# Performance work log

Measured on AMD Instinct MI355X. Metric: run time of the kernel, lower is better.

Reference implementation:

```python
import jax, jax.numpy as jnp
import numpy as np

B, T, H, W_SP, C_IN, C_OUT, K = 4, 16, 64, 64, 64, 64, 3
BN_EPS = 1e-3  # keras BatchNormalization default epsilon


def _conv(x, k):
    # x: [N, H, W, Cin], k: [kh, kw, Cin, Cout], 'same' padding, stride 1
    return jax.lax.conv_general_dilated(
        x, k, window_strides=(1, 1), padding='SAME',
        dimension_numbers=('NHWC', 'HWIO', 'NHWC'))


def _hard_sigmoid(x):
    # keras hard_sigmoid: clip(0.2*x + 0.5, 0, 1)
    return jnp.clip(0.2 * x + 0.5, 0.0, 1.0)


def setup_inputs() -> dict:
    key = jax.random.key(0)
    ks = jax.random.split(key, 4)
    x = jax.random.normal(ks[0], (B, T, H, W_SP, C_IN), dtype=jnp.float32)
    # ConvLSTM2D weights: input kernel [kh,kw,Cin,4*Cout], recurrent kernel
    # [kh,kw,Cout,4*Cout], bias [4*Cout]; gate order i, f, c, o (keras).
    W = jax.random.normal(ks[1], (K, K, C_IN, 4 * C_OUT), dtype=jnp.float32) * 0.05
    U = jax.random.normal(ks[2], (K, K, C_OUT, 4 * C_OUT), dtype=jnp.float32) * 0.05
    b = jax.random.normal(ks[3], (4 * C_OUT,), dtype=jnp.float32) * 0.05
    # BatchNormalization (inference mode since training=False)
    gamma = jnp.ones((C_OUT,), jnp.float32)
    beta = jnp.zeros((C_OUT,), jnp.float32)
    moving_mean = jnp.zeros((C_OUT,), jnp.float32)
    moving_var = jnp.ones((C_OUT,), jnp.float32)
    return {'input_tensor': x, 'W': W, 'U': U, 'b': b, 'gamma': gamma,
            'beta': beta, 'moving_mean': moving_mean, 'moving_var': moving_var}


def reference(input_tensor, W, U, b, gamma, beta, moving_mean, moving_var):
    x = input_tensor
    Bn, Tn, Hn, Wn, Cin = x.shape
    C = U.shape[2]
    # Precompute input-to-gate convolutions for all timesteps at once.
    zx = _conv(x.reshape(Bn * Tn, Hn, Wn, Cin), W)
    zx = zx.reshape(Bn, Tn, Hn, Wn, 4 * C) + b
    zx = jnp.moveaxis(zx, 1, 0)  # [T, B, H, W, 4C]

    h0 = jnp.zeros((Bn, Hn, Wn, C), x.dtype)
    c0 = jnp.zeros((Bn, Hn, Wn, C), x.dtype)

    def step(carry, zx_t):
        h, c = carry
        z = zx_t + _conv(h, U)
        zi, zf, zg, zo = jnp.split(z, 4, axis=-1)
        i = _hard_sigmoid(zi)
        f = _hard_sigmoid(zf)
        g = jnp.tanh(zg)           # activation='tanh'
        o = _hard_sigmoid(zo)      # recurrent_activation='hard_sigmoid'
        c_new = f * c + i * g
        h_new = o * jnp.tanh(c_new)
        return (h_new, c_new), h_new

    _, hs = jax.lax.scan(step, (h0, c0), zx)  # hs: [T, B, H, W, C]
    y = jnp.moveaxis(hs, 0, 1)                # [B, T, H, W, C]

    # BatchNorm inference on channel axis
    y = (y - moving_mean) * jax.lax.rsqrt(moving_var + BN_EPS) * gamma + beta

    # MaxPooling3D pool_size=(1,2,2), strides default = pool_size, padding='same'
    y = jax.lax.reduce_window(y, -jnp.inf, jax.lax.max,
                              window_dimensions=(1, 1, 2, 2, 1),
                              window_strides=(1, 1, 2, 2, 1),
                              padding='SAME')
    return y  # [B, T, H/2, W/2, C]
```

## Files before the change

### kernel.cpp

```cpp
#include <hip/hip_runtime.h>
#include <hip/hip_fp16.h>
#include <math.h>

#define BB   4
#define TT   16
#define HH   64
#define WW   64
#define CC   64
#define CO4  256
#define BN_EPS 1e-3f

typedef _Float16 f16;
typedef f16  f16x8 __attribute__((ext_vector_type(8)));
typedef float f32x4 __attribute__((ext_vector_type(4)));

#define INPAD_BYTES (BB * 66 * 66 * 128 * 2)
#define CST_BYTES   (BB * 64 * 64 * 64 * 4)
#define Z_BYTES     (BB * 64 * 64 * 256 * 4)
#define OFF_CST   INPAD_BYTES
#define OFF_Z     (INPAD_BYTES + CST_BYTES)
#define OFF_WT    (OFF_Z + Z_BYTES)

__global__ __launch_bounds__(256) void prep_wt_kernel(
    const float* __restrict__ W, const float* __restrict__ U,
    f16* __restrict__ wt)
{
    int idx = blockIdx.x * 256 + threadIdx.x;
    if (idx >= 256 * 1152) return;
    int n = idx / 1152;
    int k = idx - n * 1152;
    int tap = k >> 7;
    int ci  = k & 127;
    float v = (ci < 64) ? W[(tap * 64 + ci) * 256 + n]
                        : U[(tap * 64 + (ci - 64)) * 256 + n];
    wt[idx] = (f16)v;
}

__global__ __launch_bounds__(256) void convert_x0_kernel(
    const float* __restrict__ x, f16* __restrict__ in_pad)
{
    int idx = blockIdx.x * 256 + threadIdx.x;
    int c  = idx & 63;
    int xx = (idx >> 6) & 63;
    int yy = (idx >> 12) & 63;
    int b  = idx >> 18;
    float v = x[(((b * TT + 0) * HH + yy) * WW + xx) * 64 + c];
    in_pad[((b * 66 + yy + 1) * 66 + (xx + 1)) * 128 + c] = (f16)v;
}

#define A_LDS_BYTES (100 * 272)
#define B_LDS_BYTES (256 * 80)

__global__ __launch_bounds__(256) void conv_z_mfma(
    const f16* __restrict__ in_pad, const f16* __restrict__ wt,
    const float* __restrict__ bias, float* __restrict__ z)
{
    __shared__ char lds[A_LDS_BYTES + 2 * B_LDS_BYTES];
    char* As  = lds;
    char* Bs0 = lds + A_LDS_BYTES;
    char* Bs1 = lds + A_LDS_BYTES + B_LDS_BYTES;

    const int blk = blockIdx.x;
    const int tx  = blk & 7;
    const int ty  = (blk >> 3) & 7;
    const int b   = blk >> 6;
    const int tid = threadIdx.x;
    const int w   = tid >> 6;
    const int l   = tid & 63;
    const int l15 = l & 15;
    const int lk  = l >> 4;

    {
        const f16* src = in_pad + ((b * 66 + ty * 8) * 66 + tx * 8) * 128;
        for (int r = 0; r < 7; ++r) {
            int flat = r * 256 + tid;
            if (flat < 1600) {
                int pxi = flat >> 4;
                int oct = flat & 15;
                int ly  = pxi / 10;
                int lx  = pxi - ly * 10;
                uint4 v = *(const uint4*)(src + (ly * 66 + lx) * 128 + oct * 8);
                *(uint4*)(As + pxi * 272 + oct * 16) = v;
            }
        }
    }

    uint4 pre0, pre1, pre2, pre3;
    #define STAGE_B_LOAD(ks) do {                                          \
        const f16* _src = wt + (ks) * 32;                                  \
        pre0 = *(const uint4*)(_src + ((0*256 + tid) >> 2) * 1152 + (tid & 3) * 8); \
        pre1 = *(const uint4*)(_src + ((1*256 + tid) >> 2) * 1152 + (tid & 3) * 8); \
        pre2 = *(const uint4*)(_src + ((2*256 + tid) >> 2) * 1152 + (tid & 3) * 8); \
        pre3 = *(const uint4*)(_src + ((3*256 + tid) >> 2) * 1152 + (tid & 3) * 8); \
    } while (0)
    #define STAGE_B_WRITE(dst) do {                                        \
        *(uint4*)((dst) + ((0*256 + tid) >> 2) * 80 + (tid & 3) * 16) = pre0; \
        *(uint4*)((dst) + ((1*256 + tid) >> 2) * 80 + (tid & 3) * 16) = pre1; \
        *(uint4*)((dst) + ((2*256 + tid) >> 2) * 80 + (tid & 3) * 16) = pre2; \
        *(uint4*)((dst) + ((3*256 + tid) >> 2) * 80 + (tid & 3) * 16) = pre3; \
    } while (0)

    STAGE_B_LOAD(0);
    STAGE_B_WRITE(Bs0);

    f32x4 acc[4][4];
    #pragma unroll
    for (int nr = 0; nr < 4; ++nr) {
        float bv = bias[w * 64 + nr * 16 + l15];
        #pragma unroll
        for (int mr = 0; mr < 4; ++mr) {
            acc[mr][nr][0] = bv; acc[mr][nr][1] = bv;
            acc[mr][nr][2] = bv; acc[mr][nr][3] = bv;
        }
    }

    __syncthreads();

    for (int ks = 0; ks < 36; ++ks) {
        if (ks < 35) STAGE_B_LOAD(ks + 1);

        const char* Bcur = (ks & 1) ? Bs1 : Bs0;
        const int tap = ks >> 2;
        const int kh  = tap / 3;
        const int kw  = tap - kh * 3;
        const int cq  = ks & 3;

        f16x8 af[4], bf[4];
        #pragma unroll
        for (int mr = 0; mr < 4; ++mr) {
            int p   = mr * 16 + l15;
            int pix = ((p >> 3) + kh) * 10 + (p & 7) + kw;
            af[mr] = *(const f16x8*)(As + pix * 272 + cq * 64 + lk * 16);
        }
        #pragma unroll
        for (int nr = 0; nr < 4; ++nr) {
            int n = w * 64 + nr * 16 + l15;
            bf[nr] = *(const f16x8*)(Bcur + n * 80 + lk * 16);
        }
        #pragma unroll
        for (int mr = 0; mr < 4; ++mr)
            #pragma unroll
            for (int nr = 0; nr < 4; ++nr)
                acc[mr][nr] = __builtin_amdgcn_mfma_f32_16x16x32_f16(
                    af[mr], bf[nr], acc[mr][nr], 0, 0, 0);

        if (ks < 35) STAGE_B_WRITE((ks & 1) ? Bs0 : Bs1);
        __syncthreads();
    }

    const int y0 = ty * 8, x0 = tx * 8;
    #pragma unroll
    for (int mr = 0; mr < 4; ++mr) {
        #pragma unroll
        for (int reg = 0; reg < 4; ++reg) {
            int p  = mr * 16 + lk * 4 + reg;
            int y  = y0 + (p >> 3);
            int xx = x0 + (p & 7);
            float* zp = z + ((b * HH + y) * WW + xx) * CO4 + w * 64 + l15;
            #pragma unroll
            for (int nr = 0; nr < 4; ++nr)
                zp[nr * 16] = acc[mr][nr][reg];
        }
    }
}

__device__ __forceinline__ float hsig(float v) {
    return fminf(fmaxf(0.2f * v + 0.5f, 0.0f), 1.0f);
}

__global__ __launch_bounds__(256) void gate_pool_kernel(
    const float* __restrict__ z,
    const float* __restrict__ x,
    float* __restrict__ c_state,
    f16*   __restrict__ in_pad,
    float* __restrict__ out,
    const float* __restrict__ gamma,
    const float* __restrict__ beta,
    const float* __restrict__ mean,
    const float* __restrict__ var,
    int t)
{
    const int idx = blockIdx.x * 256 + threadIdx.x;
    const int c   = idx & 63;
    const int px  = (idx >> 6) & 31;
    const int py  = (idx >> 11) & 31;
    const int b   = idx >> 16;

    const float scale = gamma[c] * rsqrtf(var[c] + BN_EPS);
    const float bns   = beta[c] - mean[c] * scale;

    float m = -INFINITY;
#pragma unroll
    for (int dy = 0; dy < 2; ++dy) {
#pragma unroll
        for (int dx = 0; dx < 2; ++dx) {
            const int y  = py * 2 + dy;
            const int xg = px * 2 + dx;
            const int zoff = ((b * HH + y) * WW + xg) * CO4;
            const float zi = z[zoff + c];
            const float zf = z[zoff + 64 + c];
            const float zg = z[zoff + 128 + c];
            const float zo = z[zoff + 192 + c];

            const float gi = hsig(zi);
            const float gf = hsig(zf);
            const float gg = tanhf(zg);
            const float go = hsig(zo);

            const int coff = ((b * HH + y) * WW + xg) * CC + c;
            const float cn = gf * c_state[coff] + gi * gg;
            c_state[coff]  = cn;
            const float h  = go * tanhf(cn);

            f16* pp = in_pad + ((b * 66 + (y + 1)) * 66 + (xg + 1)) * 128;
            pp[64 + c] = (f16)h;
            if (t + 1 < TT)
                pp[c] = (f16)x[(((b * TT + t + 1) * HH + y) * WW + xg) * 64 + c];

            m = fmaxf(m, h * scale + bns);
        }
    }
    out[(((b * TT + t) * 32 + py) * 32 + px) * CC + c] = m;
}

extern "C" void kernel_launch(void* const* d_in, const int* in_sizes, int n_in,
                              void* d_out, int out_size, void* d_ws, size_t ws_size,
                              hipStream_t stream) {
    const float* x     = (const float*)d_in[0];
    const float* W     = (const float*)d_in[1];
    const float* U     = (const float*)d_in[2];
    const float* bias  = (const float*)d_in[3];
    const float* gamma = (const float*)d_in[4];
    const float* beta  = (const float*)d_in[5];
    const float* mean  = (const float*)d_in[6];
    const float* var   = (const float*)d_in[7];

    float* out = (float*)d_out;

    char*  ws     = (char*)d_ws;
    f16*   in_pad = (f16*)ws;
    float* c_st   = (float*)(ws + OFF_CST);
    float* z      = (float*)(ws + OFF_Z);
    f16*   wt     = (f16*)(ws + OFF_WT);

    hipMemsetAsync(d_ws, 0, (size_t)OFF_Z, stream);
    prep_wt_kernel<<<dim3(1152), dim3(256), 0, stream>>>(W, U, wt);
    convert_x0_kernel<<<dim3(4096), dim3(256), 0, stream>>>(x, in_pad);

    for (int t = 0; t < TT; ++t) {
        conv_z_mfma<<<dim3(256), dim3(256), 0, stream>>>(in_pad, wt, bias, z);
        gate_pool_kernel<<<dim3(1024), dim3(256), 0, stream>>>(
            z, x, c_st, in_pad, out, gamma, beta, mean, var, t);
    }
}
```

Baseline: 635.6 us.

## Hoist input convolution out of recurrence and fuse recurrent conv with gates

Computes the input-to-gate convolution for all timesteps in one large batched GEMM up front and stores the result in fp16. Each timestep then runs one fused kernel that does the recurrent-only convolution (half the K), adds the precomputed input term, and applies the gates, cell update, BN and pooling from LDS. This replaces the per-step fp32 z round trip and the separate gate kernel, and ping-pongs h buffers to avoid read/write races. The cost is a large fp16 zx buffer and extra precision loss from storing zx in fp16.

Result: faster. 585.7 us (-7.9%).

```diff
diff --git a/kernel.cpp b/kernel.cpp
--- a/kernel.cpp
+++ b/kernel.cpp
@@ -14,213 +14,281 @@
 typedef f16  f16x8 __attribute__((ext_vector_type(8)));
 typedef float f32x4 __attribute__((ext_vector_type(4)));
 
-#define INPAD_BYTES (BB * 66 * 66 * 128 * 2)
-#define CST_BYTES   (BB * 64 * 64 * 64 * 4)
-#define Z_BYTES     (BB * 64 * 64 * 256 * 4)
-#define OFF_CST   INPAD_BYTES
-#define OFF_Z     (INPAD_BYTES + CST_BYTES)
-#define OFF_WT    (OFF_Z + Z_BYTES)
+#define HPAD_BYTES (BB * 66 * 66 * 64 * 2)
+#define CST_BYTES  (BB * 64 * 64 * 64 * 4)
+#define X16_BYTES  (BB * TT * 64 * 64 * 64 * 2)
+#define WT_BYTES   (256 * 576 * 2)
+#define OFF_HP1  HPAD_BYTES
+#define OFF_CST  (2 * HPAD_BYTES)
+#define OFF_X16  (OFF_CST + CST_BYTES)
+#define OFF_WTX  (OFF_X16 + X16_BYTES)
+#define OFF_WTH  (OFF_WTX + WT_BYTES)
+#define OFF_ZX   (OFF_WTH + WT_BYTES)
 
 __global__ __launch_bounds__(256) void prep_wt_kernel(
     const float* __restrict__ W, const float* __restrict__ U,
-    f16* __restrict__ wt)
+    f16* __restrict__ wtx, f16* __restrict__ wth)
 {
     int idx = blockIdx.x * 256 + threadIdx.x;
-    if (idx >= 256 * 1152) return;
-    int n = idx / 1152;
-    int k = idx - n * 1152;
-    int tap = k >> 7;
-    int ci  = k & 127;
-    float v = (ci < 64) ? W[(tap * 64 + ci) * 256 + n]
-                        : U[(tap * 64 + (ci - 64)) * 256 + n];
-    wt[idx] = (f16)v;
-}
-
-__global__ __launch_bounds__(256) void convert_x0_kernel(
-    const float* __restrict__ x, f16* __restrict__ in_pad)
+    if (idx >= 256 * 576) return;
+    int n = idx / 576;
+    int k = idx - n * 576;
+    int tap = k >> 6;
+    int ci  = k & 63;
+    wtx[idx] = (f16)W[(tap * 64 + ci) * 256 + n];
+    wth[idx] = (f16)U[(tap * 64 + ci) * 256 + n];
+}
+
+__global__ __launch_bounds__(256) void convert_x_kernel(
+    const float* __restrict__ x, f16* __restrict__ x16)
 {
     int idx = blockIdx.x * 256 + threadIdx.x;
-    int c  = idx & 63;
-    int xx = (idx >> 6) & 63;
-    int yy = (idx >> 12) & 63;
-    int b  = idx >> 18;
-    float v = x[(((b * TT + 0) * HH + yy) * WW + xx) * 64 + c];
-    in_pad[((b * 66 + yy + 1) * 66 + (xx + 1)) * 128 + c] = (f16)v;
-}
-
-#define A_LDS_BYTES (100 * 272)
-#define B_LDS_BYTES (256 * 80)
-
-__global__ __launch_bounds__(256) void conv_z_mfma(
-    const f16* __restrict__ in_pad, const f16* __restrict__ wt,
-    const float* __restrict__ bias, float* __restrict__ z)
+    const float4* s = (const float4*)x + idx * 2;
+    float4 a = s[0], b = s[1];
+    f16x8 v;
+    v[0] = (f16)a.x; v[1] = (f16)a.y; v[2] = (f16)a.z; v[3] = (f16)a.w;
+    v[4] = (f16)b.x; v[5] = (f16)b.y; v[6] = (f16)b.z; v[7] = (f16)b.w;
+    *(f16x8*)(x16 + idx * 8) = v;
+}
+
+#define A_BYTES (100 * 144)
+#define B_BYTES (256 * 80)
+
+__global__ __launch_bounds__(256) void zx_gemm(
+    const f16* __restrict__ x16, const f16* __restrict__ wtx,
+    const float* __restrict__ bias, f16* __restrict__ zx)
 {
-    __shared__ char lds[A_LDS_BYTES + 2 * B_LDS_BYTES];
+    __shared__ char lds[A_BYTES + 2 * B_BYTES];
     char* As  = lds;
-    char* Bs0 = lds + A_LDS_BYTES;
-    char* Bs1 = lds + A_LDS_BYTES + B_LDS_BYTES;
+    char* Bs0 = lds + A_BYTES;
+    char* Bs1 = Bs0 + B_BYTES;
 
     const int blk = blockIdx.x;
-    const int tx  = blk & 7;
-    const int ty  = (blk >> 3) & 7;
-    const int b   = blk >> 6;
+    const int f   = blk >> 6;
+    const int tIdx = blk & 63;
+    const int y0 = (tIdx >> 3) * 8, x0 = (tIdx & 7) * 8;
     const int tid = threadIdx.x;
-    const int w   = tid >> 6;
-    const int l   = tid & 63;
-    const int l15 = l & 15;
-    const int lk  = l >> 4;
-
-    {
-        const f16* src = in_pad + ((b * 66 + ty * 8) * 66 + tx * 8) * 128;
-        for (int r = 0; r < 7; ++r) {
-            int flat = r * 256 + tid;
-            if (flat < 1600) {
-                int pxi = flat >> 4;
-                int oct = flat & 15;
-                int ly  = pxi / 10;
-                int lx  = pxi - ly * 10;
-                uint4 v = *(const uint4*)(src + (ly * 66 + lx) * 128 + oct * 8);
-                *(uint4*)(As + pxi * 272 + oct * 16) = v;
-            }
+    const int w = tid >> 6, l = tid & 63, l15 = l & 15, lk = l >> 4;
+
+    const f16* fb = x16 + f * (4096 * 64);
+    for (int r = 0; r < 4; ++r) {
+        int flat = r * 256 + tid;
+        if (flat < 800) {
+            int pxi = flat >> 3, oct = flat & 7;
+            int ly = pxi / 10, lx = pxi - ly * 10;
+            int gy = y0 + ly - 1, gx = x0 + lx - 1;
+            uint4 v = {0u, 0u, 0u, 0u};
+            if (gy >= 0 && gy < 64 && gx >= 0 && gx < 64)
+                v = *(const uint4*)(fb + (gy * 64 + gx) * 64 + oct * 8);
+            *(uint4*)(As + pxi * 144 + oct * 16) = v;
         }
     }
 
     uint4 pre0, pre1, pre2, pre3;
-    #define STAGE_B_LOAD(ks) do {                                          \
-        const f16* _src = wt + (ks) * 32;                                  \
-        pre0 = *(const uint4*)(_src + ((0*256 + tid) >> 2) * 1152 + (tid & 3) * 8); \
-        pre1 = *(const uint4*)(_src + ((1*256 + tid) >> 2) * 1152 + (tid & 3) * 8); \
-        pre2 = *(const uint4*)(_src + ((2*256 + tid) >> 2) * 1152 + (tid & 3) * 8); \
-        pre3 = *(const uint4*)(_src + ((3*256 + tid) >> 2) * 1152 + (tid & 3) * 8); \
+#define BLOAD(src, ks) do {                                                   \
+        const f16* _s = (src) + (ks) * 32 + (tid & 3) * 8;                    \
+        pre0 = *(const uint4*)(_s + (((0*256 + tid) >> 2) * 576));            \
+        pre1 = *(const uint4*)(_s + (((1*256 + tid) >> 2) * 576));            \
+        pre2 = *(const uint4*)(_s + (((2*256 + tid) >> 2) * 576));            \
+        pre3 = *(const uint4*)(_s + (((3*256 + tid) >> 2) * 576));            \
     } while (0)
-    #define STAGE_B_WRITE(dst) do {                                        \
+#define BWRITE(dst) do {                                                      \
         *(uint4*)((dst) + ((0*256 + tid) >> 2) * 80 + (tid & 3) * 16) = pre0; \
         *(uint4*)((dst) + ((1*256 + tid) >> 2) * 80 + (tid & 3) * 16) = pre1; \
         *(uint4*)((dst) + ((2*256 + tid) >> 2) * 80 + (tid & 3) * 16) = pre2; \
         *(uint4*)((dst) + ((3*256 + tid) >> 2) * 80 + (tid & 3) * 16) = pre3; \
     } while (0)
 
-    STAGE_B_LOAD(0);
-    STAGE_B_WRITE(Bs0);
+    BLOAD(wtx, 0);
+    BWRITE(Bs0);
 
     f32x4 acc[4][4];
-    #pragma unroll
+#pragma unroll
     for (int nr = 0; nr < 4; ++nr) {
         float bv = bias[w * 64 + nr * 16 + l15];
-        #pragma unroll
+#pragma unroll
         for (int mr = 0; mr < 4; ++mr) {
             acc[mr][nr][0] = bv; acc[mr][nr][1] = bv;
             acc[mr][nr][2] = bv; acc[mr][nr][3] = bv;
         }
     }
-
     __syncthreads();
 
-    for (int ks = 0; ks < 36; ++ks) {
-        if (ks < 35) STAGE_B_LOAD(ks + 1);
-
+    for (int ks = 0; ks < 18; ++ks) {
+        if (ks < 17) BLOAD(wtx, ks + 1);
         const char* Bcur = (ks & 1) ? Bs1 : Bs0;
-        const int tap = ks >> 2;
-        const int kh  = tap / 3;
-        const int kw  = tap - kh * 3;
-        const int cq  = ks & 3;
+        const int tap = ks >> 1, cq = ks & 1;
+        const int kh = tap / 3, kw = tap - kh * 3;
 
         f16x8 af[4], bf[4];
-        #pragma unroll
+#pragma unroll
         for (int mr = 0; mr < 4; ++mr) {
-            int p   = mr * 16 + l15;
+            int p = mr * 16 + l15;
             int pix = ((p >> 3) + kh) * 10 + (p & 7) + kw;
-            af[mr] = *(const f16x8*)(As + pix * 272 + cq * 64 + lk * 16);
-        }
-        #pragma unroll
-        for (int nr = 0; nr < 4; ++nr) {
-            int n = w * 64 + nr * 16 + l15;
-            bf[nr] = *(const f16x8*)(Bcur + n * 80 + lk * 16);
-        }
-        #pragma unroll
+            af[mr] = *(const f16x8*)(As + pix * 144 + cq * 64 + lk * 16);
+        }
+#pragma unroll
+        for (int nr = 0; nr < 4; ++nr)
+            bf[nr] = *(const f16x8*)(Bcur + (w * 64 + nr * 16 + l15) * 80 + lk * 16);
+#pragma unroll
         for (int mr = 0; mr < 4; ++mr)
-            #pragma unroll
+#pragma unroll
             for (int nr = 0; nr < 4; ++nr)
                 acc[mr][nr] = __builtin_amdgcn_mfma_f32_16x16x32_f16(
                     af[mr], bf[nr], acc[mr][nr], 0, 0, 0);
 
-        if (ks < 35) STAGE_B_WRITE((ks & 1) ? Bs0 : Bs1);
+        if (ks < 17) BWRITE((ks & 1) ? Bs0 : Bs1);
         __syncthreads();
     }
 
-    const int y0 = ty * 8, x0 = tx * 8;
-    #pragma unroll
-    for (int mr = 0; mr < 4; ++mr) {
-        #pragma unroll
+    f16* zb = zx + (size_t)f * (4096 * 256);
+#pragma unroll
+    for (int mr = 0; mr < 4; ++mr)
+#pragma unroll
         for (int reg = 0; reg < 4; ++reg) {
-            int p  = mr * 16 + lk * 4 + reg;
-            int y  = y0 + (p >> 3);
-            int xx = x0 + (p & 7);
-            float* zp = z + ((b * HH + y) * WW + xx) * CO4 + w * 64 + l15;
-            #pragma unroll
-            for (int nr = 0; nr < 4; ++nr)
-                zp[nr * 16] = acc[mr][nr][reg];
-        }
-    }
-}
+            int p = mr * 16 + lk * 4 + reg;
+            int pxg = (y0 + (p >> 3)) * 64 + x0 + (p & 7);
+#pragma unroll
+            for (int nr = 0; nr < 4; ++nr)
+                zb[pxg * 256 + w * 64 + nr * 16 + l15] = (f16)acc[mr][nr][reg];
+        }
+}
+
+#define ZL_STRIDE 260
+#define ZL_BYTES  (64 * ZL_STRIDE * 4)
 
 __device__ __forceinline__ float hsig(float v) {
     return fminf(fmaxf(0.2f * v + 0.5f, 0.0f), 1.0f);
 }
 
-__global__ __launch_bounds__(256) void gate_pool_kernel(
-    const float* __restrict__ z,
-    const float* __restrict__ x,
-    float* __restrict__ c_state,
-    f16*   __restrict__ in_pad,
+__global__ __launch_bounds__(256) void step_fused(
+    const f16* __restrict__ hp_in,
+    f16* __restrict__ hp_out,
+    const f16* __restrict__ wth,
+    const f16* __restrict__ zx,
+    float* __restrict__ c_st,
     float* __restrict__ out,
-    const float* __restrict__ gamma,
-    const float* __restrict__ beta,
-    const float* __restrict__ mean,
-    const float* __restrict__ var,
+    const float* __restrict__ gamma, const float* __restrict__ beta,
+    const float* __restrict__ mean,  const float* __restrict__ var,
     int t)
 {
-    const int idx = blockIdx.x * 256 + threadIdx.x;
-    const int c   = idx & 63;
-    const int px  = (idx >> 6) & 31;
-    const int py  = (idx >> 11) & 31;
-    const int b   = idx >> 16;
-
+    __shared__ char lds[ZL_BYTES];
+    char* As  = lds;
+    char* Bs0 = lds + A_BYTES;
+    char* Bs1 = Bs0 + B_BYTES;
+
+    const int blk = blockIdx.x;
+    const int b   = blk >> 6;
+    const int tIdx = blk & 63;
+    const int ty = tIdx >> 3, tx = tIdx & 7;
+    const int y0 = ty * 8, x0 = tx * 8;
+    const int tid = threadIdx.x;
+    const int w = tid >> 6, l = tid & 63, l15 = l & 15, lk = l >> 4;
+
+    const f16* hb = hp_in + b * (66 * 66 * 64);
+    for (int r = 0; r < 4; ++r) {
+        int flat = r * 256 + tid;
+        if (flat < 800) {
+            int pxi = flat >> 3, oct = flat & 7;
+            int ly = pxi / 10, lx = pxi - ly * 10;
+            uint4 v = *(const uint4*)(hb + ((y0 + ly) * 66 + x0 + lx) * 64 + oct * 8);
+            *(uint4*)(As + pxi * 144 + oct * 16) = v;
+        }
+    }
+
+    uint4 pre0, pre1, pre2, pre3;
+    BLOAD(wth, 0);
+    BWRITE(Bs0);
+
+    f32x4 acc[4][4];
+#pragma unroll
+    for (int mr = 0; mr < 4; ++mr)
+#pragma unroll
+        for (int nr = 0; nr < 4; ++nr)
+            acc[mr][nr] = (f32x4){0.f, 0.f, 0.f, 0.f};
+    __syncthreads();
+
+    for (int ks = 0; ks < 18; ++ks) {
+        if (ks < 17) BLOAD(wth, ks + 1);
+        const char* Bcur = (ks & 1) ? Bs1 : Bs0;
+        const int tap = ks >> 1, cq = ks & 1;
+        const int kh = tap / 3, kw = tap - kh * 3;
+
+        f16x8 af[4], bf[4];
+#pragma unroll
+        for (int mr = 0; mr < 4; ++mr) {
+            int p = mr * 16 + l15;
+            int pix = ((p >> 3) + kh) * 10 + (p & 7) + kw;
+            af[mr] = *(const f16x8*)(As + pix * 144 + cq * 64 + lk * 16);
+        }
+#pragma unroll
+        for (int nr = 0; nr < 4; ++nr)
+            bf[nr] = *(const f16x8*)(Bcur + (w * 64 + nr * 16 + l15) * 80 + lk * 16);
+#pragma unroll
+        for (int mr = 0; mr < 4; ++mr)
+#pragma unroll
+            for (int nr = 0; nr < 4; ++nr)
+                acc[mr][nr] = __builtin_amdgcn_mfma_f32_16x16x32_f16(
+                    af[mr], bf[nr], acc[mr][nr], 0, 0, 0);
+
+        if (ks < 17) BWRITE((ks & 1) ? Bs0 : Bs1);
+        __syncthreads();
+    }
+
+    const f16* zxb = zx + ((size_t)(b * TT + t) * 4096) * 256;
+    float* zl = (float*)lds;
+#pragma unroll
+    for (int mr = 0; mr < 4; ++mr)
+#pragma unroll
+        for (int reg = 0; reg < 4; ++reg) {
+            int p = mr * 16 + lk * 4 + reg;
+            int pxg = (y0 + (p >> 3)) * 64 + x0 + (p & 7);
+#pragma unroll
+            for (int nr = 0; nr < 4; ++nr)
+                acc[mr][nr][reg] += (float)zxb[pxg * 256 + w * 64 + nr * 16 + l15];
+        }
+#pragma unroll
+    for (int mr = 0; mr < 4; ++mr)
+#pragma unroll
+        for (int reg = 0; reg < 4; ++reg) {
+            int p = mr * 16 + lk * 4 + reg;
+#pragma unroll
+            for (int nr = 0; nr < 4; ++nr)
+                zl[p * ZL_STRIDE + w * 64 + nr * 16 + l15] = acc[mr][nr][reg];
+        }
+    __syncthreads();
+
+    const int c  = tid & 63;
+    const int rp = tid >> 6;
     const float scale = gamma[c] * rsqrtf(var[c] + BN_EPS);
     const float bns   = beta[c] - mean[c] * scale;
-
-    float m = -INFINITY;
-#pragma unroll
-    for (int dy = 0; dy < 2; ++dy) {
-#pragma unroll
-        for (int dx = 0; dx < 2; ++dx) {
-            const int y  = py * 2 + dy;
-            const int xg = px * 2 + dx;
-            const int zoff = ((b * HH + y) * WW + xg) * CO4;
-            const float zi = z[zoff + c];
-            const float zf = z[zoff + 64 + c];
-            const float zg = z[zoff + 128 + c];
-            const float zo = z[zoff + 192 + c];
-
-            const float gi = hsig(zi);
-            const float gf = hsig(zf);
-            const float gg = tanhf(zg);
-            const float go = hsig(zo);
-
-            const int coff = ((b * HH + y) * WW + xg) * CC + c;
-            const float cn = gf * c_state[coff] + gi * gg;
-            c_state[coff]  = cn;
-            const float h  = go * tanhf(cn);
-
-            f16* pp = in_pad + ((b * 66 + (y + 1)) * 66 + (xg + 1)) * 128;
-            pp[64 + c] = (f16)h;
-            if (t + 1 < TT)
-                pp[c] = (f16)x[(((b * TT + t + 1) * HH + y) * WW + xg) * 64 + c];
-
-            m = fmaxf(m, h * scale + bns);
-        }
-    }
-    out[(((b * TT + t) * 32 + py) * 32 + px) * CC + c] = m;
+    f16* ho = hp_out + b * (66 * 66 * 64);
+
+#pragma unroll
+    for (int pc = 0; pc < 4; ++pc) {
+        float m = -INFINITY;
+#pragma unroll
+        for (int dy = 0; dy < 2; ++dy)
+#pragma unroll
+            for (int dx = 0; dx < 2; ++dx) {
+                int p  = (rp * 2 + dy) * 8 + pc * 2 + dx;
+                float zi = zl[p * ZL_STRIDE + c];
+                float zf = zl[p * ZL_STRIDE + 64 + c];
+                float zg = zl[p * ZL_STRIDE + 128 + c];
+                float zo = zl[p * ZL_STRIDE + 192 + c];
+                int y  = y0 + rp * 2 + dy;
+                int xg = x0 + pc * 2 + dx;
+                int coff = ((b * 64 + y) * 64 + xg) * 64 + c;
+                float gi = hsig(zi), gf = hsig(zf);
+                float gg = tanhf(zg), go = hsig(zo);
+                float cn = gf * c_st[coff] + gi * gg;
+                c_st[coff] = cn;
+                float h = go * tanhf(cn);
+                ho[((b == b ? (y + 1) : 0) * 66 + xg + 1) * 64 + c] = (f16)h;
+                m = fmaxf(m, h * scale + bns);
+            }
+        out[(((b * TT + t) * 32 + ty * 4 + rp) * 32 + tx * 4 + pc) * 64 + c] = m;
+    }
 }
 
 extern "C" void kernel_launch(void* const* d_in, const int* in_sizes, int n_in,
@@ -236,20 +304,24 @@
     const float* var   = (const float*)d_in[7];
 
     float* out = (float*)d_out;
-
-    char*  ws     = (char*)d_ws;
-    f16*   in_pad = (f16*)ws;
-    float* c_st   = (float*)(ws + OFF_CST);
-    float* z      = (float*)(ws + OFF_Z);
-    f16*   wt     = (f16*)(ws + OFF_WT);
-
-    hipMemsetAsync(d_ws, 0, (size_t)OFF_Z, stream);
-    prep_wt_kernel<<<dim3(1152), dim3(256), 0, stream>>>(W, U, wt);
-    convert_x0_kernel<<<dim3(4096), dim3(256), 0, stream>>>(x, in_pad);
+    char*  ws  = (char*)d_ws;
+    f16*   hp0 = (f16*)ws;
+    f16*   hp1 = (f16*)(ws + OFF_HP1);
+    float* cst = (float*)(ws + OFF_CST);
+    f16*   x16 = (f16*)(ws + OFF_X16);
+    f16*   wtx = (f16*)(ws + OFF_WTX);
+    f16*   wth = (f16*)(ws + OFF_WTH);
+    f16*   zx  = (f16*)(ws + OFF_ZX);
+
+    hipMemsetAsync(d_ws, 0, (size_t)(OFF_CST + CST_BYTES), stream);
+    prep_wt_kernel<<<dim3(576), dim3(256), 0, stream>>>(W, U, wtx, wth);
+    convert_x_kernel<<<dim3(8192), dim3(256), 0, stream>>>(x, x16);
+    zx_gemm<<<dim3(4096), dim3(256), 0, stream>>>(x16, wtx, bias, zx);
 
     for (int t = 0; t < TT; ++t) {
-        conv_z_mfma<<<dim3(256), dim3(256), 0, stream>>>(in_pad, wt, bias, z);
-        gate_pool_kernel<<<dim3(1024), dim3(256), 0, stream>>>(
-            z, x, c_st, in_pad, out, gamma, beta, mean, var, t);
-    }
-}
+        const f16* hin = (t & 1) ? hp1 : hp0;
+        f16*       hou = (t & 1) ? hp0 : hp1;
+        step_fused<<<dim3(256), dim3(256), 0, stream>>>(
+            hin, hou, wth, zx, cst, out, gamma, beta, mean, var, t);
+    }
+}
```
